# Kernel optimization log

Hardware: AMD Instinct MI355X
Metric: run time of the kernel (lower is better)

The kernel has to match this reference:

```python
import jax, jax.numpy as jnp
import numpy as np

N_NODES = 50000
N_EDGES = 800000
H = 4


def setup_inputs() -> dict:
    key = jax.random.key(0)
    ks = jax.random.split(key, 12)
    s = 0.05
    return {
        "x_feat": jax.random.normal(ks[0], (N_NODES, 128), jnp.float32),
        "W_fc": jax.random.normal(ks[1], (128, 256), jnp.float32) * s,
        "W1": jax.random.normal(ks[2], (256, 256), jnp.float32) * s,
        "al1": jax.random.normal(ks[3], (H, 64), jnp.float32) * s,
        "ar1": jax.random.normal(ks[4], (H, 64), jnp.float32) * s,
        "b1": jnp.zeros((256,), jnp.float32),
        "W2": jax.random.normal(ks[5], (256, 256), jnp.float32) * s,
        "al2": jax.random.normal(ks[6], (H, 64), jnp.float32) * s,
        "ar2": jax.random.normal(ks[7], (H, 64), jnp.float32) * s,
        "b2": jnp.zeros((256,), jnp.float32),
        "src": jax.random.randint(ks[8], (N_EDGES,), 0, N_NODES, jnp.int64 if jax.config.jax_enable_x64 else jnp.int32),
        "dst": jax.random.randint(ks[9], (N_EDGES,), 0, N_NODES, jnp.int64 if jax.config.jax_enable_x64 else jnp.int32),
    }


def _gat_layer(x, src, dst, W, attn_l, attn_r, bias, n_nodes):
    """DGL GATConv: project, per-edge leaky-relu scores, edge softmax by dst,
    weighted segment-sum, + bias, ELU. Returns [N, H, dh]."""
    h, dh = attn_l.shape
    feat = (x @ W).reshape(n_nodes, h, dh)            # [N,H,dh]
    el = jnp.einsum('nhd,hd->nh', feat, attn_l)        # [N,H]
    er = jnp.einsum('nhd,hd->nh', feat, attn_r)        # [N,H]
    e = jax.nn.leaky_relu(el[src] + er[dst], 0.2)      # [E,H]
    # numerically stable segment softmax over incoming edges of each dst
    m = jax.ops.segment_max(e, dst, num_segments=n_nodes)
    ex = jnp.exp(e - m[dst])
    z = jax.ops.segment_sum(ex, dst, num_segments=n_nodes)
    a = ex / z[dst]                                    # [E,H]
    msg = feat[src] * a[:, :, None]                    # [E,H,dh]
    out = jax.ops.segment_sum(msg, dst, num_segments=n_nodes)  # [N,H,dh]
    out = out + bias.reshape(h, dh)
    return jax.nn.elu(out)


def reference(x_feat, W_fc, W1, al1, ar1, b1, W2, al2, ar2, b2, src, dst):
    n = x_feat.shape[0]
    h = jnp.tanh(x_feat @ W_fc)                         # [N,256] (dropout = identity in eval)
    g1 = _gat_layer(h, src, dst, W1, al1, ar1, b1, n)   # [N,4,64]
    g1 = g1.reshape(n, -1)                              # [N,256]
    g2 = _gat_layer(g1, src, dst, W2, al2, ar2, b2, n)  # [N,4,64]
    return jnp.mean(g2, axis=-2)                        # mean over heads -> [N,64]
```

## Files before the change

kernel.cpp:

```cpp
#include <hip/hip_runtime.h>
#include <hip/hip_bf16.h>
#include <hip/hip_fp16.h>
#include <math.h>


typedef __attribute__((ext_vector_type(8))) short bf16x8;
typedef __attribute__((ext_vector_type(4))) float f32x4;

typedef const __attribute__((address_space(1))) char gas_char;
typedef __attribute__((address_space(3))) char las_char;

__device__ __forceinline__ void gload16(const void* g, void* l) {
    __builtin_amdgcn_global_load_lds((gas_char*)g, (las_char*)l, 16, 0, 0);
}

__device__ __forceinline__ void split2(float v, short& h, short& l) {
    __hip_bfloat16 bh = __float2bfloat16(v);
    float r = v - __bfloat162float(bh);
    __hip_bfloat16 bl = __float2bfloat16(r);
    h = *reinterpret_cast<short*>(&bh);
    l = *reinterpret_cast<short*>(&bl);
}

__device__ __forceinline__ float fast_tanh(float x) {
    x = fminf(fmaxf(x, -15.f), 15.f);
    float e = __expf(2.f * x);
    return (e - 1.f) * __builtin_amdgcn_rcpf(e + 1.f);
}

__device__ __forceinline__ float leaky02(float x) { return x > 0.f ? x : 0.2f * x; }

__device__ __forceinline__ float sel_head(float4 q, int h) {
    float lo = (h & 1) ? q.y : q.x;
    float hi = (h & 1) ? q.w : q.z;
    return (h & 2) ? hi : lo;
}

__global__ __launch_bounds__(256) void prep_kernel(
        const float* __restrict__ X, short* __restrict__ Xh, short* __restrict__ Xl,
        int xquads,
        const float* __restrict__ W0, short* __restrict__ B0h, short* __restrict__ B0l,
        const float* __restrict__ W1, short* __restrict__ B1h, short* __restrict__ B1l,
        const float* __restrict__ W2, short* __restrict__ B2h, short* __restrict__ B2l,
        int* __restrict__ deg, int N) {
    int gid = blockIdx.x * 256 + threadIdx.x;
    if (gid < N) deg[gid] = 0;
    if (gid < xquads) {
        float4 v = reinterpret_cast<const float4*>(X)[gid];
        short4 h, l;
        split2(v.x, h.x, l.x);
        split2(v.y, h.y, l.y);
        split2(v.z, h.z, l.z);
        split2(v.w, h.w, l.w);
        reinterpret_cast<short4*>(Xh)[gid] = h;
        reinterpret_cast<short4*>(Xl)[gid] = l;
        return;
    }
    int rel = gid - xquads;
    const float* W;
    short *Bh, *Bl;
    int K;
    if (rel < 128 * 256) {
        W = W0; Bh = B0h; Bl = B0l; K = 128;
    } else if (rel < 128 * 256 + 256 * 256) {
        W = W1; Bh = B1h; Bl = B1l; K = 256; rel -= 128 * 256;
    } else if (rel < 128 * 256 + 2 * 256 * 256) {
        W = W2; Bh = B2h; Bl = B2l; K = 256; rel -= 128 * 256 + 256 * 256;
    } else {
        return;
    }
    int k = rel >> 8, n = rel & 255;
    short h, l;
    split2(W[rel], h, l);
    Bh[n * K + k] = h;
    Bl[n * K + k] = l;
}

template<int K, bool TANH, bool ELER, bool SPLIT_OUT>
__global__ __launch_bounds__(256, 2) void mfma_gemm_kernel(
        const short* __restrict__ Ah, const short* __restrict__ Al,
        const short* __restrict__ Bh, const short* __restrict__ Bl,
        short* __restrict__ Oh, short* __restrict__ Ol, __half* __restrict__ O16,
        int M,
        const float* __restrict__ al, const float* __restrict__ ar,
        float* __restrict__ el, float* __restrict__ er) {
    __shared__ __align__(16) short As_h[2][128 * 32];
    __shared__ __align__(16) short As_l[2][128 * 32];
    __shared__ __align__(16) short Bs_h[2][128 * 32];
    __shared__ __align__(16) short Bs_l[2][128 * 32];

    const int tid = threadIdx.x;
    const int row0 = blockIdx.x * 128;
    const int col0 = blockIdx.y * 128;

    const int lane = tid & 63;
    const int lr = lane & 15;
    const int lg = lane >> 4;
    const int wid = tid >> 6;
    const int wm = wid >> 1;
    const int wn = wid & 1;

    const int srow = wid * 32 + (lane >> 2);
    const int scol = (lane & 3) * 8;
    const size_t aoff1 = (size_t)(row0 + srow) * K + scol;
    const size_t aoff2 = aoff1 + (size_t)16 * K;
    const size_t boff1 = (size_t)(col0 + srow) * K + scol;
    const size_t boff2 = boff1 + (size_t)16 * K;
    const int lbase1 = (wid * 32) * 32;
    const int lbase2 = (wid * 32 + 16) * 32;

    auto stage = [&](int buf, int k0) {
        gload16(Ah + aoff1 + k0, &As_h[buf][lbase1]);
        gload16(Ah + aoff2 + k0, &As_h[buf][lbase2]);
        gload16(Al + aoff1 + k0, &As_l[buf][lbase1]);
        gload16(Al + aoff2 + k0, &As_l[buf][lbase2]);
        gload16(Bh + boff1 + k0, &Bs_h[buf][lbase1]);
        gload16(Bh + boff2 + k0, &Bs_h[buf][lbase2]);
        gload16(Bl + boff1 + k0, &Bs_l[buf][lbase1]);
        gload16(Bl + boff2 + k0, &Bs_l[buf][lbase2]);
    };

    f32x4 acc[4][4];
#pragma unroll
    for (int i = 0; i < 4; ++i)
#pragma unroll
        for (int j = 0; j < 4; ++j) acc[i][j] = (f32x4){0.f, 0.f, 0.f, 0.f};

    constexpr int NT = K / 32;
    stage(0, 0);
    __syncthreads();

    int cur = 0;
#pragma unroll
    for (int t = 0; t < NT; ++t) {
        if (t + 1 < NT) stage(cur ^ 1, (t + 1) * 32);

        bf16x8 ah[4], av[4], bh[4], bv[4];
#pragma unroll
        for (int q = 0; q < 4; ++q) {
            int arow = (wm * 64 + q * 16 + lr) * 32 + lg * 8;
            int brow = (wn * 64 + q * 16 + lr) * 32 + lg * 8;
            ah[q] = *reinterpret_cast<const bf16x8*>(&As_h[cur][arow]);
            av[q] = *reinterpret_cast<const bf16x8*>(&As_l[cur][arow]);
            bh[q] = *reinterpret_cast<const bf16x8*>(&Bs_h[cur][brow]);
            bv[q] = *reinterpret_cast<const bf16x8*>(&Bs_l[cur][brow]);
        }
#pragma unroll
        for (int mt = 0; mt < 4; ++mt)
#pragma unroll
            for (int nt = 0; nt < 4; ++nt) {
                acc[mt][nt] = __builtin_amdgcn_mfma_f32_16x16x32_bf16(ah[mt], bh[nt], acc[mt][nt], 0, 0, 0);
                acc[mt][nt] = __builtin_amdgcn_mfma_f32_16x16x32_bf16(ah[mt], bv[nt], acc[mt][nt], 0, 0, 0);
                acc[mt][nt] = __builtin_amdgcn_mfma_f32_16x16x32_bf16(av[mt], bh[nt], acc[mt][nt], 0, 0, 0);
            }
        __syncthreads();
        cur ^= 1;
    }

    const int head = blockIdx.y * 2 + wn;
    float alv[4], arv[4];
    if (ELER) {
#pragma unroll
        for (int nt = 0; nt < 4; ++nt) {
            alv[nt] = al[head * 64 + nt * 16 + lr];
            arv[nt] = ar[head * 64 + nt * 16 + lr];
        }
    }
#pragma unroll
    for (int mt = 0; mt < 4; ++mt) {
#pragma unroll
        for (int r = 0; r < 4; ++r) {
            int row = row0 + wm * 64 + mt * 16 + lg * 4 + r;
            bool valid = row < M;
            float sl = 0.f, sr_ = 0.f;
#pragma unroll
            for (int nt = 0; nt < 4; ++nt) {
                float v = acc[mt][nt][r];
                if (TANH) v = fast_tanh(v);
                if (valid) {
                    size_t ci = (size_t)row * 256 + col0 + wn * 64 + nt * 16 + lr;
                    if (SPLIT_OUT) {
                        short hh, ll;
                        split2(v, hh, ll);
                        Oh[ci] = hh;
                        Ol[ci] = ll;
                    } else {
                        O16[ci] = __float2half(v);
                    }
                }
                if (ELER) { sl = fmaf(v, alv[nt], sl); sr_ = fmaf(v, arv[nt], sr_); }
            }
            if (ELER) {
#pragma unroll
                for (int mask = 1; mask < 16; mask <<= 1) {
                    sl  += __shfl_xor(sl, mask, 16);
                    sr_ += __shfl_xor(sr_, mask, 16);
                }
                if (valid && lr == 0) {
                    el[row * 4 + head] = sl;
                    er[row * 4 + head] = sr_;
                }
            }
        }
    }
}

__global__ void count_deg_kernel(const int* __restrict__ dst, int* __restrict__ deg, int E) {
    int i = blockIdx.x * blockDim.x + threadIdx.x;
    if (i < E) atomicAdd(&deg[dst[i]], 1);
}

__global__ __launch_bounds__(1024) void scan_kernel(const int* __restrict__ deg,
                                                    int* __restrict__ offs,
                                                    int* __restrict__ cursor, int n) {
    __shared__ int wsum[16];
    const int tid = threadIdx.x, lane = tid & 63, wv = tid >> 6;
    int carry = 0;
    for (int base = 0; base < n; base += 4096) {
        int i = base + tid * 4;
        int v0 = 0, v1 = 0, v2 = 0, v3 = 0;
        if (i + 3 < n) {
            int4 q = *reinterpret_cast<const int4*>(&deg[i]);
            v0 = q.x; v1 = q.y; v2 = q.z; v3 = q.w;
        } else if (i < n) {
            v0 = deg[i];
            if (i + 1 < n) v1 = deg[i + 1];
            if (i + 2 < n) v2 = deg[i + 2];
        }
        int s = v0 + v1 + v2 + v3;
        int incl = s;
#pragma unroll
        for (int d = 1; d < 64; d <<= 1) {
            int t = __shfl_up(incl, d, 64);
            if (lane >= d) incl += t;
        }
        if (lane == 63) wsum[wv] = incl;
        __syncthreads();
        int woff = 0, tot = 0;
#pragma unroll
        for (int w2 = 0; w2 < 16; ++w2) {
            int x = wsum[w2];
            if (w2 < wv) woff += x;
            tot += x;
        }
        int excl = carry + woff + incl - s;
        if (i < n) {
            int p0 = excl, p1 = p0 + v0, p2 = p1 + v1, p3 = p2 + v2;
            offs[i] = p0; cursor[i] = p0;
            if (i + 1 < n) { offs[i + 1] = p1; cursor[i + 1] = p1; }
            if (i + 2 < n) { offs[i + 2] = p2; cursor[i + 2] = p2; }
            if (i + 3 < n) { offs[i + 3] = p3; cursor[i + 3] = p3; }
        }
        carry += tot;
        __syncthreads();
    }
    if (tid == 0) offs[n] = carry;
}

__global__ void fill_csr_kernel(const int* __restrict__ src, const int* __restrict__ dst,
                                int* __restrict__ cursor, int* __restrict__ srcs_sorted, int E) {
    int i = blockIdx.x * blockDim.x + threadIdx.x;
    if (i < E) {
        int d = dst[i];
        int pos = atomicAdd(&cursor[d], 1);
        srcs_sorted[pos] = src[i];
    }
}

template<bool FINAL>
__global__ __launch_bounds__(256) void gat_agg_kernel(const __half* __restrict__ feat,
                                                      const float* __restrict__ el,
                                                      const float* __restrict__ er,
                                                      const int* __restrict__ srcs,
                                                      const int* __restrict__ offs,
                                                      const float* __restrict__ bias,
                                                      float* __restrict__ out,
                                                      short* __restrict__ Gh,
                                                      short* __restrict__ Gl, int N) {
    const int tid = threadIdx.x;
    const int w = tid >> 6, l = tid & 63;
    const int n = blockIdx.x * 4 + w;
    if (n >= N) return;
    const int h = l >> 4;
    const int begin = offs[n];
    const int deg = offs[n + 1] - begin;
    const float erh = er[n * 4 + h];
    const __half* fbase = feat + (size_t)l * 4;

    float4 acc = make_float4(0.f, 0.f, 0.f, 0.f);
    float z = 0.f;

    for (int j = 0; j < deg; j += 8) {
        const int rem = deg - j;
        const int nb = __builtin_amdgcn_readfirstlane(begin + j);
        const int s0 = srcs[nb + 0];
        const int s1 = (rem > 1) ? srcs[nb + 1] : 0;
        const int s2 = (rem > 2) ? srcs[nb + 2] : 0;
        const int s3 = (rem > 3) ? srcs[nb + 3] : 0;
        const int s4 = (rem > 4) ? srcs[nb + 4] : 0;
        const int s5 = (rem > 5) ? srcs[nb + 5] : 0;
        const int s6 = (rem > 6) ? srcs[nb + 6] : 0;
        const int s7 = (rem > 7) ? srcs[nb + 7] : 0;
        const float4 q0 = *reinterpret_cast<const float4*>(&el[(size_t)s0 * 4]);
        const float4 q1 = *reinterpret_cast<const float4*>(&el[(size_t)s1 * 4]);
        const float4 q2 = *reinterpret_cast<const float4*>(&el[(size_t)s2 * 4]);
        const float4 q3 = *reinterpret_cast<const float4*>(&el[(size_t)s3 * 4]);
        const float4 q4 = *reinterpret_cast<const float4*>(&el[(size_t)s4 * 4]);
        const float4 q5 = *reinterpret_cast<const float4*>(&el[(size_t)s5 * 4]);
        const float4 q6 = *reinterpret_cast<const float4*>(&el[(size_t)s6 * 4]);
        const float4 q7 = *reinterpret_cast<const float4*>(&el[(size_t)s7 * 4]);
        const uint2 u0 = *reinterpret_cast<const uint2*>(fbase + (size_t)s0 * 256);
        const uint2 u1 = *reinterpret_cast<const uint2*>(fbase + (size_t)s1 * 256);
        const uint2 u2 = *reinterpret_cast<const uint2*>(fbase + (size_t)s2 * 256);
        const uint2 u3 = *reinterpret_cast<const uint2*>(fbase + (size_t)s3 * 256);
        const uint2 u4 = *reinterpret_cast<const uint2*>(fbase + (size_t)s4 * 256);
        const uint2 u5 = *reinterpret_cast<const uint2*>(fbase + (size_t)s5 * 256);
        const uint2 u6 = *reinterpret_cast<const uint2*>(fbase + (size_t)s6 * 256);
        const uint2 u7 = *reinterpret_cast<const uint2*>(fbase + (size_t)s7 * 256);

        const float e0 = __expf(leaky02(sel_head(q0, h) + erh));
        const float e1 = (rem > 1) ? __expf(leaky02(sel_head(q1, h) + erh)) : 0.f;
        const float e2 = (rem > 2) ? __expf(leaky02(sel_head(q2, h) + erh)) : 0.f;
        const float e3 = (rem > 3) ? __expf(leaky02(sel_head(q3, h) + erh)) : 0.f;
        const float e4 = (rem > 4) ? __expf(leaky02(sel_head(q4, h) + erh)) : 0.f;
        const float e5 = (rem > 5) ? __expf(leaky02(sel_head(q5, h) + erh)) : 0.f;
        const float e6 = (rem > 6) ? __expf(leaky02(sel_head(q6, h) + erh)) : 0.f;
        const float e7 = (rem > 7) ? __expf(leaky02(sel_head(q7, h) + erh)) : 0.f;
        z += ((e0 + e1) + (e2 + e3)) + ((e4 + e5) + (e6 + e7));

        auto fma4 = [&](float e, uint2 u) {
            const __half2* hp = reinterpret_cast<const __half2*>(&u);
            float2 a = __half22float2(hp[0]);
            float2 b = __half22float2(hp[1]);
            acc.x = fmaf(e, a.x, acc.x); acc.y = fmaf(e, a.y, acc.y);
            acc.z = fmaf(e, b.x, acc.z); acc.w = fmaf(e, b.y, acc.w);
        };
        fma4(e0, u0); fma4(e1, u1); fma4(e2, u2); fma4(e3, u3);
        fma4(e4, u4); fma4(e5, u5); fma4(e6, u6); fma4(e7, u7);
    }

    const float rz = (z > 0.f) ? __builtin_amdgcn_rcpf(z) : 0.f;
    const float4 bv = *reinterpret_cast<const float4*>(&bias[l * 4]);
    float4 v;
    v.x = fmaf(acc.x, rz, bv.x);
    v.y = fmaf(acc.y, rz, bv.y);
    v.z = fmaf(acc.z, rz, bv.z);
    v.w = fmaf(acc.w, rz, bv.w);
    v.x = v.x > 0.f ? v.x : expm1f(v.x);
    v.y = v.y > 0.f ? v.y : expm1f(v.y);
    v.z = v.z > 0.f ? v.z : expm1f(v.z);
    v.w = v.w > 0.f ? v.w : expm1f(v.w);

    if (!FINAL) {
        short4 hh, ll;
        split2(v.x, hh.x, ll.x);
        split2(v.y, hh.y, ll.y);
        split2(v.z, hh.z, ll.z);
        split2(v.w, hh.w, ll.w);
        *reinterpret_cast<short4*>(&Gh[(size_t)n * 256 + l * 4]) = hh;
        *reinterpret_cast<short4*>(&Gl[(size_t)n * 256 + l * 4]) = ll;
    } else {
        v.x += __shfl_down(v.x, 32, 64); v.y += __shfl_down(v.y, 32, 64);
        v.z += __shfl_down(v.z, 32, 64); v.w += __shfl_down(v.w, 32, 64);
        v.x += __shfl_down(v.x, 16, 64); v.y += __shfl_down(v.y, 16, 64);
        v.z += __shfl_down(v.z, 16, 64); v.w += __shfl_down(v.w, 16, 64);
        if (l < 16) {
            float4 o;
            o.x = 0.25f * v.x; o.y = 0.25f * v.y; o.z = 0.25f * v.z; o.w = 0.25f * v.w;
            *reinterpret_cast<float4*>(&out[(size_t)n * 64 + l * 4]) = o;
        }
    }
}

extern "C" void kernel_launch(void* const* d_in, const int* in_sizes, int n_in,
                              void* d_out, int out_size, void* d_ws, size_t ws_size,
                              hipStream_t stream) {
    const float* x_feat = (const float*)d_in[0];
    const float* W_fc   = (const float*)d_in[1];
    const float* W1     = (const float*)d_in[2];
    const float* al1    = (const float*)d_in[3];
    const float* ar1    = (const float*)d_in[4];
    const float* b1     = (const float*)d_in[5];
    const float* W2     = (const float*)d_in[6];
    const float* al2    = (const float*)d_in[7];
    const float* ar2    = (const float*)d_in[8];
    const float* b2     = (const float*)d_in[9];
    const int*   src    = (const int*)d_in[10];
    const int*   dst    = (const int*)d_in[11];
    float* out = (float*)d_out;

    const int N = in_sizes[0] / 128;
    const int E = in_sizes[10];
    const int NB = (N + 127) / 128;
    const int M_pad = NB * 128;

    char* ws = (char*)d_ws;
    size_t off = 0;
    auto alloc = [&](size_t bytes) -> void* {
        off = (off + 255) & ~(size_t)255;
        void* p = ws + off;
        off += bytes;
        return p;
    };
    short* Xh   = (short*)alloc((size_t)M_pad * 128 * 2);
    short* Xl   = (short*)alloc((size_t)M_pad * 128 * 2);
    short* Hh   = (short*)alloc((size_t)M_pad * 256 * 2);
    short* Hl   = (short*)alloc((size_t)M_pad * 256 * 2);
    __half* f16 = (__half*)alloc((size_t)M_pad * 256 * 2);
    float* el   = (float*)alloc((size_t)N * 4 * 4);
    float* er   = (float*)alloc((size_t)N * 4 * 4);
    int* deg    = (int*)alloc((size_t)N * 4);
    int* offs   = (int*)alloc((size_t)(N + 4) * 4);
    int* cursor = (int*)alloc((size_t)N * 4);
    int* srcs_sorted = (int*)alloc((size_t)(E + 8) * 4);
    short* Bfc_h = (short*)alloc((size_t)256 * 128 * 2);
    short* Bfc_l = (short*)alloc((size_t)256 * 128 * 2);
    short* B1_h  = (short*)alloc((size_t)256 * 256 * 2);
    short* B1_l  = (short*)alloc((size_t)256 * 256 * 2);
    short* B2_h  = (short*)alloc((size_t)256 * 256 * 2);
    short* B2_l  = (short*)alloc((size_t)256 * 256 * 2);

    const int eb = (E + 255) / 256;
    dim3 ggrid(NB, 2);
    const int agrid = (N + 3) / 4;

    const int xquads = N * 128 / 4;
    const int prep_threads = xquads + 128 * 256 + 2 * 256 * 256;
    prep_kernel<<<(prep_threads + 255) / 256, 256, 0, stream>>>(
        x_feat, Xh, Xl, xquads, W_fc, Bfc_h, Bfc_l, W1, B1_h, B1_l, W2, B2_h, B2_l,
        deg, N);
    count_deg_kernel<<<eb, 256, 0, stream>>>(dst, deg, E);
    scan_kernel<<<1, 1024, 0, stream>>>(deg, offs, cursor, N);
    fill_csr_kernel<<<eb, 256, 0, stream>>>(src, dst, cursor, srcs_sorted, E);
    mfma_gemm_kernel<128, true, false, true><<<ggrid, 256, 0, stream>>>(
        Xh, Xl, Bfc_h, Bfc_l, Hh, Hl, nullptr, N, nullptr, nullptr, nullptr, nullptr);
    mfma_gemm_kernel<256, false, true, false><<<ggrid, 256, 0, stream>>>(
        Hh, Hl, B1_h, B1_l, nullptr, nullptr, f16, N, al1, ar1, el, er);
    gat_agg_kernel<false><<<agrid, 256, 0, stream>>>(
        f16, el, er, srcs_sorted, offs, b1, nullptr, Hh, Hl, N);
    mfma_gemm_kernel<256, false, true, false><<<ggrid, 256, 0, stream>>>(
        Hh, Hl, B2_h, B2_l, nullptr, nullptr, f16, N, al2, ar2, el, er);
    gat_agg_kernel<true><<<agrid, 256, 0, stream>>>(
        f16, el, er, srcs_sorted, offs, b2, out, nullptr, nullptr, N);
}
```

Measured before the change: 455.6 us.

## Widen GEMM tiles to full 256 columns and fuse fp32 input split into GEMM

The GEMM now uses 512-thread blocks covering all 256 output columns per 128-row tile. Each A tile is loaded once instead of twice, and the el/er head reduction no longer depends on the grid y index. The first GEMM reads fp32 x_feat directly and splits it into bf16 hi/lo in-kernel, which removes the separate X split pass and its workspace traffic. In exchange, double buffering is dropped in favour of a load-sync-compute-sync loop, so memory latency may be less hidden. The grid is also halved, which may reduce parallelism.

```diff
diff --git a/kernel.cpp b/kernel.cpp
--- a/kernel.cpp
+++ b/kernel.cpp
@@ -37,26 +37,13 @@
 }
 
 __global__ __launch_bounds__(256) void prep_kernel(
-        const float* __restrict__ X, short* __restrict__ Xh, short* __restrict__ Xl,
-        int xquads,
         const float* __restrict__ W0, short* __restrict__ B0h, short* __restrict__ B0l,
         const float* __restrict__ W1, short* __restrict__ B1h, short* __restrict__ B1l,
         const float* __restrict__ W2, short* __restrict__ B2h, short* __restrict__ B2l,
         int* __restrict__ deg, int N) {
     int gid = blockIdx.x * 256 + threadIdx.x;
     if (gid < N) deg[gid] = 0;
-    if (gid < xquads) {
-        float4 v = reinterpret_cast<const float4*>(X)[gid];
-        short4 h, l;
-        split2(v.x, h.x, l.x);
-        split2(v.y, h.y, l.y);
-        split2(v.z, h.z, l.z);
-        split2(v.w, h.w, l.w);
-        reinterpret_cast<short4*>(Xh)[gid] = h;
-        reinterpret_cast<short4*>(Xl)[gid] = l;
-        return;
-    }
-    int rel = gid - xquads;
+    int rel = gid;
     const float* W;
     short *Bh, *Bl;
     int K;
@@ -76,49 +63,32 @@
     Bl[n * K + k] = l;
 }
 
-template<int K, bool TANH, bool ELER, bool SPLIT_OUT>
-__global__ __launch_bounds__(256, 2) void mfma_gemm_kernel(
+template<int K, bool AFP32, bool TANH, bool ELER, bool SPLIT_OUT>
+__global__ __launch_bounds__(512, 4) void mfma_gemm_kernel(
+        const float* __restrict__ Af,
         const short* __restrict__ Ah, const short* __restrict__ Al,
         const short* __restrict__ Bh, const short* __restrict__ Bl,
         short* __restrict__ Oh, short* __restrict__ Ol, __half* __restrict__ O16,
         int M,
         const float* __restrict__ al, const float* __restrict__ ar,
         float* __restrict__ el, float* __restrict__ er) {
-    __shared__ __align__(16) short As_h[2][128 * 32];
-    __shared__ __align__(16) short As_l[2][128 * 32];
-    __shared__ __align__(16) short Bs_h[2][128 * 32];
-    __shared__ __align__(16) short Bs_l[2][128 * 32];
+    __shared__ __align__(16) short As_h[128 * 32];
+    __shared__ __align__(16) short As_l[128 * 32];
+    __shared__ __align__(16) short Bs_h[256 * 32];
+    __shared__ __align__(16) short Bs_l[256 * 32];
 
     const int tid = threadIdx.x;
     const int row0 = blockIdx.x * 128;
-    const int col0 = blockIdx.y * 128;
-
     const int lane = tid & 63;
     const int lr = lane & 15;
     const int lg = lane >> 4;
     const int wid = tid >> 6;
-    const int wm = wid >> 1;
-    const int wn = wid & 1;
-
-    const int srow = wid * 32 + (lane >> 2);
-    const int scol = (lane & 3) * 8;
-    const size_t aoff1 = (size_t)(row0 + srow) * K + scol;
-    const size_t aoff2 = aoff1 + (size_t)16 * K;
-    const size_t boff1 = (size_t)(col0 + srow) * K + scol;
-    const size_t boff2 = boff1 + (size_t)16 * K;
-    const int lbase1 = (wid * 32) * 32;
-    const int lbase2 = (wid * 32 + 16) * 32;
-
-    auto stage = [&](int buf, int k0) {
-        gload16(Ah + aoff1 + k0, &As_h[buf][lbase1]);
-        gload16(Ah + aoff2 + k0, &As_h[buf][lbase2]);
-        gload16(Al + aoff1 + k0, &As_l[buf][lbase1]);
-        gload16(Al + aoff2 + k0, &As_l[buf][lbase2]);
-        gload16(Bh + boff1 + k0, &Bs_h[buf][lbase1]);
-        gload16(Bh + boff2 + k0, &Bs_h[buf][lbase2]);
-        gload16(Bl + boff1 + k0, &Bs_l[buf][lbase1]);
-        gload16(Bl + boff2 + k0, &Bs_l[buf][lbase2]);
-    };
+    const int wm = wid >> 2;
+    const int wn = wid & 3;
+
+    const int arow16 = 16 * wid + (lane >> 2);
+    const int acol = (lane & 3) * 8;
+    const int brow32 = 32 * wid + (lane >> 2);
 
     f32x4 acc[4][4];
 #pragma unroll
@@ -127,37 +97,60 @@
         for (int j = 0; j < 4; ++j) acc[i][j] = (f32x4){0.f, 0.f, 0.f, 0.f};
 
     constexpr int NT = K / 32;
-    stage(0, 0);
-    __syncthreads();
-
-    int cur = 0;
 #pragma unroll
     for (int t = 0; t < NT; ++t) {
-        if (t + 1 < NT) stage(cur ^ 1, (t + 1) * 32);
-
-        bf16x8 ah[4], av[4], bh[4], bv[4];
+        const int k0 = t * 32;
+        if (AFP32) {
+            const int row = tid >> 2;
+            const int c8 = (tid & 3) * 8;
+            int g = row0 + row;
+            float va[8];
+            if (g < M) {
+                const float4* ap = reinterpret_cast<const float4*>(&Af[(size_t)g * K + k0 + c8]);
+                *reinterpret_cast<float4*>(&va[0]) = ap[0];
+                *reinterpret_cast<float4*>(&va[4]) = ap[1];
+            } else {
+#pragma unroll
+                for (int i = 0; i < 8; ++i) va[i] = 0.f;
+            }
+            short hs[8], ls[8];
+#pragma unroll
+            for (int i = 0; i < 8; ++i) split2(va[i], hs[i], ls[i]);
+            *reinterpret_cast<bf16x8*>(&As_h[row * 32 + c8]) = *reinterpret_cast<bf16x8*>(&hs[0]);
+            *reinterpret_cast<bf16x8*>(&As_l[row * 32 + c8]) = *reinterpret_cast<bf16x8*>(&ls[0]);
+        } else {
+            gload16(Ah + (size_t)(row0 + arow16) * K + k0 + acol, &As_h[wid * 512]);
+            gload16(Al + (size_t)(row0 + arow16) * K + k0 + acol, &As_l[wid * 512]);
+        }
+        gload16(Bh + (size_t)brow32 * K + k0 + acol, &Bs_h[wid * 1024]);
+        gload16(Bh + (size_t)(brow32 + 16) * K + k0 + acol, &Bs_h[wid * 1024 + 512]);
+        gload16(Bl + (size_t)brow32 * K + k0 + acol, &Bs_l[wid * 1024]);
+        gload16(Bl + (size_t)(brow32 + 16) * K + k0 + acol, &Bs_l[wid * 1024 + 512]);
+        __syncthreads();
+
+        bf16x8 ah[4], av[4];
 #pragma unroll
         for (int q = 0; q < 4; ++q) {
             int arow = (wm * 64 + q * 16 + lr) * 32 + lg * 8;
-            int brow = (wn * 64 + q * 16 + lr) * 32 + lg * 8;
-            ah[q] = *reinterpret_cast<const bf16x8*>(&As_h[cur][arow]);
-            av[q] = *reinterpret_cast<const bf16x8*>(&As_l[cur][arow]);
-            bh[q] = *reinterpret_cast<const bf16x8*>(&Bs_h[cur][brow]);
-            bv[q] = *reinterpret_cast<const bf16x8*>(&Bs_l[cur][brow]);
-        }
-#pragma unroll
-        for (int mt = 0; mt < 4; ++mt)
-#pragma unroll
-            for (int nt = 0; nt < 4; ++nt) {
-                acc[mt][nt] = __builtin_amdgcn_mfma_f32_16x16x32_bf16(ah[mt], bh[nt], acc[mt][nt], 0, 0, 0);
-                acc[mt][nt] = __builtin_amdgcn_mfma_f32_16x16x32_bf16(ah[mt], bv[nt], acc[mt][nt], 0, 0, 0);
-                acc[mt][nt] = __builtin_amdgcn_mfma_f32_16x16x32_bf16(av[mt], bh[nt], acc[mt][nt], 0, 0, 0);
+            ah[q] = *reinterpret_cast<const bf16x8*>(&As_h[arow]);
+            av[q] = *reinterpret_cast<const bf16x8*>(&As_l[arow]);
+        }
+#pragma unroll
+        for (int nt = 0; nt < 4; ++nt) {
+            int brow = (wn * 64 + nt * 16 + lr) * 32 + lg * 8;
+            bf16x8 bh = *reinterpret_cast<const bf16x8*>(&Bs_h[brow]);
+            bf16x8 bv = *reinterpret_cast<const bf16x8*>(&Bs_l[brow]);
+#pragma unroll
+            for (int mt = 0; mt < 4; ++mt) {
+                acc[mt][nt] = __builtin_amdgcn_mfma_f32_16x16x32_bf16(ah[mt], bh, acc[mt][nt], 0, 0, 0);
+                acc[mt][nt] = __builtin_amdgcn_mfma_f32_16x16x32_bf16(ah[mt], bv, acc[mt][nt], 0, 0, 0);
+                acc[mt][nt] = __builtin_amdgcn_mfma_f32_16x16x32_bf16(av[mt], bh, acc[mt][nt], 0, 0, 0);
             }
+        }
         __syncthreads();
-        cur ^= 1;
-    }
-
-    const int head = blockIdx.y * 2 + wn;
+    }
+
+    const int head = wn;
     float alv[4], arv[4];
     if (ELER) {
 #pragma unroll
@@ -178,7 +171,7 @@
                 float v = acc[mt][nt][r];
                 if (TANH) v = fast_tanh(v);
                 if (valid) {
-                    size_t ci = (size_t)row * 256 + col0 + wn * 64 + nt * 16 + lr;
+                    size_t ci = (size_t)row * 256 + wn * 64 + nt * 16 + lr;
                     if (SPLIT_OUT) {
                         short hh, ll;
                         split2(v, hh, ll);
@@ -402,8 +395,6 @@
         off += bytes;
         return p;
     };
-    short* Xh   = (short*)alloc((size_t)M_pad * 128 * 2);
-    short* Xl   = (short*)alloc((size_t)M_pad * 128 * 2);
     short* Hh   = (short*)alloc((size_t)M_pad * 256 * 2);
     short* Hl   = (short*)alloc((size_t)M_pad * 256 * 2);
     __half* f16 = (__half*)alloc((size_t)M_pad * 256 * 2);
@@ -421,25 +412,23 @@
     short* B2_l  = (short*)alloc((size_t)256 * 256 * 2);
 
     const int eb = (E + 255) / 256;
-    dim3 ggrid(NB, 2);
     const int agrid = (N + 3) / 4;
 
-    const int xquads = N * 128 / 4;
-    const int prep_threads = xquads + 128 * 256 + 2 * 256 * 256;
+    const int prep_threads = 128 * 256 + 2 * 256 * 256;
     prep_kernel<<<(prep_threads + 255) / 256, 256, 0, stream>>>(
-        x_feat, Xh, Xl, xquads, W_fc, Bfc_h, Bfc_l, W1, B1_h, B1_l, W2, B2_h, B2_l,
-        deg, N);
+        W_fc, Bfc_h, Bfc_l, W1, B1_h, B1_l, W2, B2_h, B2_l, deg, N);
     count_deg_kernel<<<eb, 256, 0, stream>>>(dst, deg, E);
     scan_kernel<<<1, 1024, 0, stream>>>(deg, offs, cursor, N);
     fill_csr_kernel<<<eb, 256, 0, stream>>>(src, dst, cursor, srcs_sorted, E);
-    mfma_gemm_kernel<128, true, false, true><<<ggrid, 256, 0, stream>>>(
-        Xh, Xl, Bfc_h, Bfc_l, Hh, Hl, nullptr, N, nullptr, nullptr, nullptr, nullptr);
-    mfma_gemm_kernel<256, false, true, false><<<ggrid, 256, 0, stream>>>(
-        Hh, Hl, B1_h, B1_l, nullptr, nullptr, f16, N, al1, ar1, el, er);
+    mfma_gemm_kernel<128, true, true, false, true><<<NB, 512, 0, stream>>>(
+        x_feat, nullptr, nullptr, Bfc_h, Bfc_l, Hh, Hl, nullptr, N,
+        nullptr, nullptr, nullptr, nullptr);
+    mfma_gemm_kernel<256, false, false, true, false><<<NB, 512, 0, stream>>>(
+        nullptr, Hh, Hl, B1_h, B1_l, nullptr, nullptr, f16, N, al1, ar1, el, er);
     gat_agg_kernel<false><<<agrid, 256, 0, stream>>>(
         f16, el, er, srcs_sorted, offs, b1, nullptr, Hh, Hl, N);
-    mfma_gemm_kernel<256, false, true, false><<<ggrid, 256, 0, stream>>>(
-        Hh, Hl, B2_h, B2_l, nullptr, nullptr, f16, N, al2, ar2, el, er);
+    mfma_gemm_kernel<256, false, false, true, false><<<NB, 512, 0, stream>>>(
+        nullptr, Hh, Hl, B2_h, B2_l, nullptr, nullptr, f16, N, al2, ar2, el, er);
     gat_agg_kernel<true><<<agrid, 256, 0, stream>>>(
         f16, el, er, srcs_sorted, offs, b2, out, nullptr, nullptr, N);
 }
```

After: 435.4 us. 1.05x faster.
